# Kernel tuning notes

Hardware: AMD Instinct MI355X
Metric: run time of the kernel (lower is better)

Reference implementation:

```python
import jax, jax.numpy as jnp
import numpy as np

NUM_HEADS = 32
HEAD_DIM = 128
ROPE_THETA = 10000.0


def _rope_tables(seq_len, head_dim, theta):
    inv_freq = 1.0 / (theta ** (jnp.arange(0, head_dim, 2, dtype=jnp.float32) / head_dim))
    pos = jnp.arange(seq_len, dtype=jnp.float32)
    freqs = pos[:, None] * inv_freq[None, :]            # [S, hd/2]
    emb = jnp.concatenate([freqs, freqs], axis=-1)      # [S, hd]
    return jnp.cos(emb), jnp.sin(emb)


def _rotate_half(x):
    x1, x2 = jnp.split(x, 2, axis=-1)
    return jnp.concatenate([-x2, x1], axis=-1)


def _apply_rope(x, cos, sin):
    # x: [B, S, H, D]; cos/sin: [S, D] -> unsqueeze_dim=2 broadcasting
    c = cos[None, :, None, :]
    s = sin[None, :, None, :]
    return x * c + _rotate_half(x) * s


def setup_inputs() -> dict:
    key = jax.random.key(0)
    ks = jax.random.split(key, 6)
    hidden = 4096
    B, S = 2, 4096  # global sequence = world_size * local_seq (4 * 1024)
    hidden_states = jax.random.normal(ks[0], (B, S, hidden), dtype=jnp.float32)
    # original uses torch.rand (uniform); scaled by 0.02 for numerical sanity
    q_proj = jax.random.uniform(ks[1], (hidden, hidden), dtype=jnp.float32) * 0.02
    k_proj = jax.random.uniform(ks[2], (hidden, hidden), dtype=jnp.float32) * 0.02
    v_proj = jax.random.uniform(ks[3], (hidden, hidden), dtype=jnp.float32) * 0.02
    o_proj = jax.random.uniform(ks[4], (hidden, hidden), dtype=jnp.float32) * 0.02
    return {"hidden_states": hidden_states, "q_proj": q_proj, "k_proj": k_proj,
            "v_proj": v_proj, "o_proj": o_proj, "world_size": 4}


def _ring_attention(hidden_states, q_proj, k_proj, v_proj, o_proj, world_size):
    B, S, H = hidden_states.shape
    s_local = S // world_size
    nh, hd = NUM_HEADS, HEAD_DIM
    scale = 1.0 / np.sqrt(hd).astype(np.float32)

    # rank 0 holds the first sequence shard as its local hidden states
    hs_local = hidden_states[:, :s_local]
    q = (hs_local @ q_proj.T).reshape(B, s_local, nh, hd)
    k = (hidden_states @ k_proj.T).reshape(B, S, nh, hd)
    v = (hidden_states @ v_proj.T).reshape(B, S, nh, hd)

    cos, sin = _rope_tables(S, hd, ROPE_THETA)
    q = _apply_rope(q, cos[:s_local], sin[:s_local])   # rank0 positions 0..s_local-1
    k = _apply_rope(k, cos, sin)                       # global positions per shard

    # split into per-rank KV blocks; rank 0 receives blocks W-1, W-2, ..., 0
    k_blocks = k.reshape(B, world_size, s_local, nh, hd).transpose(1, 0, 2, 3, 4)[::-1]
    v_blocks = v.reshape(B, world_size, s_local, nh, hd).transpose(1, 0, 2, 3, 4)[::-1]

    def step(carry, kv):
        attn, max_lse, denom, lse_full = carry
        k_blk, v_blk = kv
        # memory_efficient_attention_partial: non-causal partial attention + lse
        s = jnp.einsum('bqhd,bkhd->bhqk', q, k_blk) * scale
        m = jnp.max(s, axis=-1)                          # [B,H,q]
        p = jnp.exp(s - m[..., None])
        l = jnp.sum(p, axis=-1)
        lse = (m + jnp.log(l)).transpose(0, 2, 1)        # [B,q,H]
        out = jnp.einsum('bhqk,bkhd->bqhd', p / l[..., None], v_blk)
        # online-softmax merge across ring steps
        new_max = jnp.maximum(max_lse, lse)
        old_adj = jnp.exp(max_lse - new_max)[..., None]
        new_adj = jnp.exp(lse - new_max)[..., None]
        denom = old_adj * denom + new_adj
        attn = old_adj * attn + new_adj * out
        lse_full = new_max + jnp.log(jnp.exp(lse_full - new_max) + jnp.exp(lse - new_max))
        return (attn, new_max, denom, lse_full), None

    init = (jnp.zeros((B, s_local, nh, hd), jnp.float32),
            jnp.full((B, s_local, nh), -jnp.inf, jnp.float32),
            jnp.zeros((B, s_local, nh, 1), jnp.float32),
            jnp.full((B, s_local, nh), -jnp.inf, jnp.float32))
    (attn, _, denom, _), _ = jax.lax.scan(step, init, (k_blocks, v_blocks))

    attn = attn / denom
    attn = attn.astype(jnp.float16).astype(jnp.float32)  # .half() in source
    attn = attn.reshape(B, s_local, nh * hd)
    return attn @ o_proj.T


def reference(hidden_states, q_proj, k_proj, v_proj, o_proj, world_size):
    return _ring_attention(hidden_states, q_proj, k_proj, v_proj, o_proj, world_size)
```

## Files before the change

kernel.cpp:

```cpp
#include <hip/hip_runtime.h>


using bf16x8 = __attribute__((ext_vector_type(8))) short;
using f32x4  = __attribute__((ext_vector_type(4))) float;

__device__ inline unsigned short f32_to_bf16_bits(float f) {
  unsigned int u = __float_as_uint(f);
  u += 0x7FFFu + ((u >> 16) & 1u);
  return (unsigned short)(u >> 16);
}
__device__ inline float bf16_bits_to_f32(unsigned short h) {
  return __uint_as_float(((unsigned int)h) << 16);
}

__device__ __forceinline__ void load_lds16(const unsigned short* g, unsigned short* l) {
  __builtin_amdgcn_global_load_lds(
      (const __attribute__((address_space(1))) void*)g,
      (__attribute__((address_space(3))) void*)l, 16, 0, 0);
}

__global__ void cast_f32_bf16(const float* __restrict__ in,
                              unsigned short* __restrict__ out, long n4) {
  long i = (long)blockIdx.x * blockDim.x + threadIdx.x;
  long stride = (long)gridDim.x * blockDim.x;
  for (; i < n4; i += stride) {
    float4 v = reinterpret_cast<const float4*>(in)[i];
    ushort4 o;
    o.x = f32_to_bf16_bits(v.x);
    o.y = f32_to_bf16_bits(v.y);
    o.z = f32_to_bf16_bits(v.z);
    o.w = f32_to_bf16_bits(v.w);
    reinterpret_cast<ushort4*>(out)[i] = o;
  }
}

__global__ void rope_tables(float* __restrict__ cos_t, float* __restrict__ sin_t) {
  int idx = blockIdx.x * 256 + threadIdx.x;
  if (idx >= 4096 * 64) return;
  int p = idx >> 6, i = idx & 63;
  float inv = __expf(-(float)i * (9.210340371976184f / 64.0f));
  float f = (float)p * inv;
  cos_t[idx] = cosf(f);
  sin_t[idx] = sinf(f);
}

__global__ void rope_apply_v(unsigned short* __restrict__ buf,
                             const float4* __restrict__ cos4,
                             const float4* __restrict__ sin4,
                             long nchunks, int pos_mask, float gain) {
  long idx = (long)blockIdx.x * 256 + threadIdx.x;
  if (idx >= nchunks) return;
  long tok = idx >> 8;
  int rem = (int)(idx & 255);
  int head = rem >> 3, c = rem & 7;
  int pos = (int)(tok & (long)pos_mask);
  float4 ct0 = cos4[pos * 16 + c * 2];
  float4 ct1 = cos4[pos * 16 + c * 2 + 1];
  float4 st0 = sin4[pos * 16 + c * 2];
  float4 st1 = sin4[pos * 16 + c * 2 + 1];
  float cs[8] = {ct0.x, ct0.y, ct0.z, ct0.w, ct1.x, ct1.y, ct1.z, ct1.w};
  float sn[8] = {st0.x, st0.y, st0.z, st0.w, st1.x, st1.y, st1.z, st1.w};
  long base = tok * 4096 + head * 128 + c * 8;
  bf16x8 x1 = *reinterpret_cast<const bf16x8*>(buf + base);
  bf16x8 x2 = *reinterpret_cast<const bf16x8*>(buf + base + 64);
  bf16x8 o1, o2;
#pragma unroll
  for (int j = 0; j < 8; j++) {
    float a = bf16_bits_to_f32((unsigned short)x1[j]);
    float b = bf16_bits_to_f32((unsigned short)x2[j]);
    o1[j] = (short)f32_to_bf16_bits((a * cs[j] - b * sn[j]) * gain);
    o2[j] = (short)f32_to_bf16_bits((b * cs[j] + a * sn[j]) * gain);
  }
  *reinterpret_cast<bf16x8*>(buf + base) = o1;
  *reinterpret_cast<bf16x8*>(buf + base + 64) = o2;
}

__device__ inline void storeC(float* p, float v) { *p = v; }
__device__ inline void storeC(unsigned short* p, float v) { *p = f32_to_bf16_bits(v); }

template <typename OUT_T>
__global__ __launch_bounds__(256) void gemm_bt(const unsigned short* __restrict__ A,
                                               const unsigned short* __restrict__ B,
                                               OUT_T* __restrict__ C,
                                               long Astride_z, long Cstride_z, int N) {
  __shared__ unsigned short As[128 * 32];
  __shared__ unsigned short Bs[128 * 32];
  const int tid = threadIdx.x;
  const int bn = blockIdx.x, bm = blockIdx.y, bz = blockIdx.z;
  const unsigned short* Ab = A + (long)bz * Astride_z + (long)bm * 128 * 4096;
  const unsigned short* Bb = B + (long)bn * 128 * 4096;
  OUT_T* Cb = C + (long)bz * Cstride_z + (long)bm * 128 * N + (long)bn * 128;

  const int lane = tid & 63;
  const int w = tid >> 6;
  const int wr = (w >> 1) * 64, wc = (w & 1) * 64;
  const int fr = lane & 15, fg = lane >> 4;

  f32x4 acc[4][4] = {};

  const int c0 = tid, c1 = tid + 256;
  const int rA0 = c0 >> 2, kc0 = c0 & 3;
  const int rA1 = c1 >> 2, kc1 = c1 & 3;

  for (int k0 = 0; k0 < 4096; k0 += 32) {
    load_lds16(Ab + (long)rA0 * 4096 + k0 + kc0 * 8, As + c0 * 8);
    load_lds16(Ab + (long)rA1 * 4096 + k0 + kc1 * 8, As + c1 * 8);
    load_lds16(Bb + (long)rA0 * 4096 + k0 + kc0 * 8, Bs + c0 * 8);
    load_lds16(Bb + (long)rA1 * 4096 + k0 + kc1 * 8, Bs + c1 * 8);
    __syncthreads();
    bf16x8 af[4], bfv[4];
#pragma unroll
    for (int m = 0; m < 4; m++)
      af[m] = *reinterpret_cast<const bf16x8*>(As + (wr + m * 16 + fr) * 32 + fg * 8);
#pragma unroll
    for (int n = 0; n < 4; n++)
      bfv[n] = *reinterpret_cast<const bf16x8*>(Bs + (wc + n * 16 + fr) * 32 + fg * 8);
#pragma unroll
    for (int m = 0; m < 4; m++)
#pragma unroll
      for (int n = 0; n < 4; n++)
        acc[m][n] = __builtin_amdgcn_mfma_f32_16x16x32_bf16(af[m], bfv[n], acc[m][n], 0, 0, 0);
    __syncthreads();
  }
#pragma unroll
  for (int m = 0; m < 4; m++)
#pragma unroll
    for (int n = 0; n < 4; n++)
#pragma unroll
      for (int r = 0; r < 4; r++) {
        int row = wr + m * 16 + fg * 4 + r;
        int col = wc + n * 16 + fr;
        storeC(Cb + (long)row * N + col, acc[m][n][r]);
      }
}

#define STG2(Gb, Lb, h, kc)                                                    \
  load_lds16((Gb) + (long)((h) * 128 + srow) * 4096 + sslot * 8 + (kc),        \
             (Lb) + tid * 8);                                                  \
  load_lds16((Gb) + (long)((h) * 128 + 64 + srow) * 4096 + sslot * 8 + (kc),   \
             (Lb) + 4096 + tid * 8);

#define MFMAQ(MH, NH)                                                          \
  _Pragma("unroll") for (int mi = 0; mi < 4; ++mi)                             \
    _Pragma("unroll") for (int ni = 0; ni < 2; ++ni)                           \
      _Pragma("unroll") for (int kk = 0; kk < 2; ++kk)                         \
        acc[(MH) * 4 + mi][(NH) * 2 + ni] =                                    \
            __builtin_amdgcn_mfma_f32_16x16x32_bf16(                           \
                a[mi][kk], b[(NH) * 2 + ni][kk],                               \
                acc[(MH) * 4 + mi][(NH) * 2 + ni], 0, 0, 0);

#define TILE(P, KC, MODE)                                                      \
  {                                                                            \
    const unsigned short* Ar = lds + wm * 16384 + (P) * 8192;                  \
    const unsigned short* Br =                                                 \
        lds + 32768 + (wn >> 1) * 16384 + (P) * 8192 + (wn & 1) * 4096;        \
    _Pragma("unroll") for (int mf = 0; mf < 4; ++mf) {                         \
      a[mf][0] = *reinterpret_cast<const bf16x8*>(Ar + mf * 1024 + ao0);       \
      a[mf][1] = *reinterpret_cast<const bf16x8*>(Ar + mf * 1024 + ao1);       \
    }                                                                          \
    _Pragma("unroll") for (int nf = 0; nf < 2; ++nf) {                         \
      b[nf][0] = *reinterpret_cast<const bf16x8*>(Br + nf * 1024 + ao0);       \
      b[nf][1] = *reinterpret_cast<const bf16x8*>(Br + nf * 1024 + ao1);       \
    }                                                                          \
    __builtin_amdgcn_s_setprio(1);                                             \
    MFMAQ(0, 0);                                                               \
    __builtin_amdgcn_s_setprio(0);                                             \
    _Pragma("unroll") for (int nf = 2; nf < 4; ++nf) {                         \
      b[nf][0] = *reinterpret_cast<const bf16x8*>(Br + nf * 1024 + ao0);       \
      b[nf][1] = *reinterpret_cast<const bf16x8*>(Br + nf * 1024 + ao1);       \
    }                                                                          \
    __builtin_amdgcn_s_setprio(1);                                             \
    MFMAQ(0, 1);                                                               \
    __builtin_amdgcn_s_setprio(0);                                             \
    asm volatile("s_waitcnt lgkmcnt(0)" ::: "memory");                         \
    asm volatile("s_barrier" ::: "memory");            \
    if ((MODE) == 0) {                                                         \
      STG2(Bg, lds + 32768 + (P) * 8192, 0, KC);                               \
      STG2(Bg, lds + 49152 + (P) * 8192, 1, KC);                               \
    }                                                                          \
    _Pragma("unroll") for (int mf = 0; mf < 4; ++mf) {                         \
      a[mf][0] = *reinterpret_cast<const bf16x8*>(Ar + (4 + mf) * 1024 + ao0); \
      a[mf][1] = *reinterpret_cast<const bf16x8*>(Ar + (4 + mf) * 1024 + ao1); \
    }                                                                          \
    __builtin_amdgcn_s_setprio(1);                                             \
    MFMAQ(1, 0);                                                               \
    __builtin_amdgcn_s_setprio(0);                                             \
    asm volatile("s_waitcnt lgkmcnt(0)" ::: "memory");                         \
    asm volatile("s_barrier" ::: "memory");            \
    if ((MODE) == 0) {                                                         \
      STG2(Ag, lds + (P) * 8192, 0, KC);                                       \
      STG2(Ag, lds + 16384 + (P) * 8192, 1, KC);                               \
    }                                                                          \
    __builtin_amdgcn_s_setprio(1);                                             \
    MFMAQ(1, 1);                                                               \
    __builtin_amdgcn_s_setprio(0);                                             \
    if ((MODE) == 0) asm volatile("s_waitcnt vmcnt(8)" ::: "memory");          \
    if ((MODE) == 1) asm volatile("s_waitcnt vmcnt(0)" ::: "memory");          \
    asm volatile("s_barrier" ::: "memory");       \
  }

template <typename OUT_T>
__global__ __launch_bounds__(512, 2) void gemm256(const unsigned short* __restrict__ A,
                                                  const unsigned short* __restrict__ B,
                                                  OUT_T* __restrict__ C,
                                                  long Astride_z, long Cstride_z, int N) {
  __shared__ unsigned short lds[65536];
  const int tid = threadIdx.x;
  const int bn = blockIdx.x, bm = blockIdx.y, bz = blockIdx.z;
  const unsigned short* Ag = A + (long)bz * Astride_z + (long)bm * 256 * 4096;
  const unsigned short* Bg = B + (long)bn * 256 * 4096;

  const int w = tid >> 6, lane = tid & 63;
  const int wm = w >> 2, wn = w & 3;
  const int fr = lane & 15, fg = lane >> 4;
  const int ao0 = fr * 64 + ((fg ^ (fr & 7)) * 8);
  const int ao1 = fr * 64 + (((4 + fg) ^ (fr & 7)) * 8);
  const int srow = tid >> 3;
  const int sslot = (tid & 7) ^ (srow & 7);

  f32x4 acc[8][4] = {};
  bf16x8 a[4][2], b[4][2];

  STG2(Ag, lds + 0, 0, 0);     STG2(Ag, lds + 16384, 1, 0);
  STG2(Bg, lds + 32768, 0, 0); STG2(Bg, lds + 49152, 1, 0);
  STG2(Ag, lds + 8192, 0, 64);  STG2(Ag, lds + 24576, 1, 64);
  STG2(Bg, lds + 40960, 0, 64); STG2(Bg, lds + 57344, 1, 64);
  asm volatile("s_waitcnt vmcnt(8)" ::: "memory");
  asm volatile("s_barrier" ::: "memory");

  for (int ti = 0; ti < 31; ++ti) {
    TILE(0, (2 * ti + 2) * 64, 0);
    TILE(1, (2 * ti + 3) * 64, 0);
  }
  TILE(0, 0, 1);
  TILE(1, 0, 2);

  OUT_T* Cb = C + (long)bz * Cstride_z + ((long)bm * 256) * N + bn * 256;
#pragma unroll
  for (int mf = 0; mf < 8; ++mf)
#pragma unroll
    for (int nf = 0; nf < 4; ++nf)
#pragma unroll
      for (int rr = 0; rr < 4; ++rr) {
        int row = wm * 128 + mf * 16 + fg * 4 + rr;
        int col = wn * 64 + nf * 16 + fr;
        storeC(Cb + (long)row * N + col, acc[mf][nf][rr]);
      }
}

#define AT_STAGE(P, kv)                                                        \
  _Pragma("unroll") for (int i = 0; i < 4; i++) {                              \
    int c = tid + 256 * i;                                                     \
    int key = c >> 4, s0 = c & 15;                                             \
    int Lg = s0 ^ (key & 15);                                                  \
    load_lds16(kbase + (long)((kv) + key) * 4096 + Lg * 8, &Ks[P][c * 8]);     \
  }                                                                            \
  _Pragma("unroll") for (int i = 0; i < 4; i++) {                              \
    int c = tid + 256 * i;                                                     \
    int f0 = c >> 3, s0 = c & 7;                                               \
    int Lg = s0 ^ (f0 & 7);                                                    \
    load_lds16(vbase + (long)f0 * 8192 + (kv) + Lg * 8, &Vl[P][c * 8]);        \
  }

__global__ __launch_bounds__(256) void attn_fwd(const unsigned short* __restrict__ qb,
                                                const unsigned short* __restrict__ kb,
                                                const unsigned short* __restrict__ vT,
                                                unsigned short* __restrict__ ob) {
  __shared__ unsigned short Ks[2][64 * 128];
  __shared__ unsigned short Vl[2][128 * 64];
  __shared__ unsigned short Ps[4][16 * 72];

  const int qt = blockIdx.x, h = blockIdx.y, b = blockIdx.z;
  const int tid = threadIdx.x, w = tid >> 6, lane = tid & 63;
  const int fr = lane & 15, fg = lane >> 4;

  const unsigned short* kbase = kb + (long)b * 4096 * 4096 + h * 128;
  const unsigned short* vbase = vT + (long)h * 128 * 8192 + (long)b * 4096;

  bf16x8 qf[4];
  {
    const unsigned short* qptr =
        qb + ((long)b * 1024 + qt * 64 + w * 16 + fr) * 4096 + h * 128 + fg * 8;
#pragma unroll
    for (int c = 0; c < 4; c++) qf[c] = *reinterpret_cast<const bf16x8*>(qptr + c * 32);
  }

  f32x4 outa[8] = {};
  float m_run[4], l_run[4];
#pragma unroll
  for (int r = 0; r < 4; r++) { m_run[r] = -1e30f; l_run[r] = 0.0f; }

  AT_STAGE(0, 0);
  asm volatile("s_waitcnt vmcnt(0)" ::: "memory");
  asm volatile("s_barrier" ::: "memory");

  for (int t = 0; t < 64; ++t) {
    const int cur = t & 1;
    if (t < 63) { AT_STAGE(cur ^ 1, (t + 1) * 64); }

    f32x4 sacc[4];
#pragma unroll
    for (int ks = 0; ks < 4; ks++) {
      f32x4 aq = {0.f, 0.f, 0.f, 0.f};
#pragma unroll
      for (int cc = 0; cc < 4; cc++) {
        bf16x8 kf = *reinterpret_cast<const bf16x8*>(
            &Ks[cur][(ks * 16 + fr) * 128 + (((cc * 4 + fg) ^ fr) & 15) * 8]);
        aq = __builtin_amdgcn_mfma_f32_16x16x32_bf16(qf[cc], kf, aq, 0, 0, 0);
      }
      sacc[ks] = aq;
    }

    float mx4[4];
#pragma unroll
    for (int r = 0; r < 4; r++) {
      float mx = fmaxf(fmaxf(sacc[0][r], sacc[1][r]), fmaxf(sacc[2][r], sacc[3][r]));
      mx = fmaxf(mx, __shfl_xor(mx, 1));
      mx = fmaxf(mx, __shfl_xor(mx, 2));
      mx = fmaxf(mx, __shfl_xor(mx, 4));
      mx = fmaxf(mx, __shfl_xor(mx, 8));
      mx4[r] = mx;
    }
    int need = 0;
#pragma unroll
    for (int r = 0; r < 4; r++) need |= (mx4[r] > m_run[r] + 11.5f) ? 1 : 0;
    if (__any(need)) {
#pragma unroll
      for (int r = 0; r < 4; r++) {
        float mnew = fmaxf(m_run[r], mx4[r]);
        float ef = exp2f(m_run[r] - mnew);
        l_run[r] *= ef;
        m_run[r] = mnew;
#pragma unroll
        for (int ds = 0; ds < 8; ds++) outa[ds][r] *= ef;
      }
    }
#pragma unroll
    for (int r = 0; r < 4; r++) {
      float sum = 0.f;
#pragma unroll
      for (int ks = 0; ks < 4; ks++) {
        float pv = exp2f(sacc[ks][r] - m_run[r]);
        Ps[w][(fg * 4 + r) * 72 + ks * 16 + fr] = f32_to_bf16_bits(pv);
        sum += pv;
      }
      l_run[r] += sum;
    }

#pragma unroll
    for (int c2 = 0; c2 < 2; c2++) {
      bf16x8 pf = *reinterpret_cast<const bf16x8*>(&Ps[w][fr * 72 + c2 * 32 + fg * 8]);
#pragma unroll
      for (int ds = 0; ds < 8; ds++) {
        int feat = ds * 16 + fr;
        int pch = ((c2 * 4 + fg) ^ (feat & 7)) & 7;
        bf16x8 vf = *reinterpret_cast<const bf16x8*>(&Vl[cur][feat * 64 + pch * 8]);
        outa[ds] = __builtin_amdgcn_mfma_f32_16x16x32_bf16(pf, vf, outa[ds], 0, 0, 0);
      }
    }

    if (t < 63) {
      asm volatile("s_waitcnt lgkmcnt(0)" ::: "memory");
      asm volatile("s_waitcnt vmcnt(0)" ::: "memory");
      asm volatile("s_barrier" ::: "memory");
    }
  }

#pragma unroll
  for (int r = 0; r < 4; r++) {
    float l = l_run[r];
    l += __shfl_xor(l, 1);
    l += __shfl_xor(l, 2);
    l += __shfl_xor(l, 4);
    l += __shfl_xor(l, 8);
    float inv = 1.0f / l;
    unsigned short* op =
        ob + ((long)b * 1024 + qt * 64 + w * 16 + fg * 4 + r) * 4096 + h * 128;
#pragma unroll
    for (int ds = 0; ds < 8; ds++) op[ds * 16 + fr] = f32_to_bf16_bits(outa[ds][r] * inv);
  }
}

extern "C" void kernel_launch(void* const* d_in, const int* in_sizes, int n_in,
                              void* d_out, int out_size, void* d_ws, size_t ws_size,
                              hipStream_t stream) {
  const float* hs = (const float*)d_in[0];
  const float* wq = (const float*)d_in[1];
  const float* wk = (const float*)d_in[2];
  const float* wv = (const float*)d_in[3];
  const float* wo = (const float*)d_in[4];
  float* out = (float*)d_out;

  const long hsN = 2L * 4096 * 4096;
  const long wN  = 4096L * 4096;

  unsigned short* hs_b = (unsigned short*)d_ws;
  unsigned short* wq_b = hs_b + hsN;
  unsigned short* wk_b = wq_b + wN;
  unsigned short* wv_b = wk_b + wN;
  unsigned short* wo_b = wv_b + wN;
  unsigned short* q_b  = wo_b + wN;
  unsigned short* k_b  = q_b + 2048L * 4096;
  unsigned short* vT_b = k_b + 8192L * 4096;
  unsigned short* at_b = vT_b + 8192L * 4096;
  float* cos_t = (float*)(at_b + 2048L * 4096);
  float* sin_t = cos_t + 4096 * 64;

  cast_f32_bf16<<<dim3(4096), dim3(256), 0, stream>>>(hs, hs_b, hsN / 4);
  cast_f32_bf16<<<dim3(2048), dim3(256), 0, stream>>>(wq, wq_b, wN / 4);
  cast_f32_bf16<<<dim3(2048), dim3(256), 0, stream>>>(wk, wk_b, wN / 4);
  cast_f32_bf16<<<dim3(2048), dim3(256), 0, stream>>>(wv, wv_b, wN / 4);
  cast_f32_bf16<<<dim3(2048), dim3(256), 0, stream>>>(wo, wo_b, wN / 4);

  rope_tables<<<dim3(1024), dim3(256), 0, stream>>>(cos_t, sin_t);

  gemm_bt<unsigned short><<<dim3(32, 8, 2), dim3(256), 0, stream>>>(
      hs_b, wq_b, q_b, 4096L * 4096, 1024L * 4096, 4096);
  gemm256<unsigned short><<<dim3(16, 16, 2), dim3(512), 0, stream>>>(
      hs_b, wk_b, k_b, 4096L * 4096, 4096L * 4096, 4096);
  gemm256<unsigned short><<<dim3(32, 16, 1), dim3(512), 0, stream>>>(
      wv_b, hs_b, vT_b, 0L, 0L, 8192);

  const float qgain = 0.08838834764831845f * 1.4426950408889634f;
  rope_apply_v<<<dim3(2048), dim3(256), 0, stream>>>(
      q_b, (const float4*)cos_t, (const float4*)sin_t, 2048L * 256, 1023, qgain);
  rope_apply_v<<<dim3(8192), dim3(256), 0, stream>>>(
      k_b, (const float4*)cos_t, (const float4*)sin_t, 8192L * 256, 4095, 1.0f);

  attn_fwd<<<dim3(16, 32, 2), dim3(256), 0, stream>>>(q_b, k_b, vT_b, at_b);

  gemm_bt<float><<<dim3(32, 16, 1), dim3(256), 0, stream>>>(
      at_b, wo_b, out, 0L, 0L, 4096);
}
```

Baseline: 1.078 ms.

## Load V fragments directly from global into registers and defer row-max shuffles

The attention kernel stops staging V tiles through shared memory. Each wave now reads its V MFMA operands straight from global memory into registers. These loads are issued early, before the softmax, so their latency can overlap with the exp work. The per-row max shuffle reduction now runs only when some lane's local max exceeds the running max by the rescale threshold, which removes cross-lane shuffles on most iterations. This frees LDS and cuts LDS traffic and bank pressure, but each of the four waves fetches the same V block on its own, so global/L2 traffic goes up and load latency may be exposed.

```diff
diff --git a/kernel.cpp b/kernel.cpp
--- a/kernel.cpp
+++ b/kernel.cpp
@@ -248,18 +248,12 @@
       }
 }
 
-#define AT_STAGE(P, kv)                                                        \
+#define KSTAGE(P, kv)                                                          \
   _Pragma("unroll") for (int i = 0; i < 4; i++) {                              \
     int c = tid + 256 * i;                                                     \
     int key = c >> 4, s0 = c & 15;                                             \
     int Lg = s0 ^ (key & 15);                                                  \
     load_lds16(kbase + (long)((kv) + key) * 4096 + Lg * 8, &Ks[P][c * 8]);     \
-  }                                                                            \
-  _Pragma("unroll") for (int i = 0; i < 4; i++) {                              \
-    int c = tid + 256 * i;                                                     \
-    int f0 = c >> 3, s0 = c & 7;                                               \
-    int Lg = s0 ^ (f0 & 7);                                                    \
-    load_lds16(vbase + (long)f0 * 8192 + (kv) + Lg * 8, &Vl[P][c * 8]);        \
   }
 
 __global__ __launch_bounds__(256) void attn_fwd(const unsigned short* __restrict__ qb,
@@ -267,7 +261,6 @@
                                                 const unsigned short* __restrict__ vT,
                                                 unsigned short* __restrict__ ob) {
   __shared__ unsigned short Ks[2][64 * 128];
-  __shared__ unsigned short Vl[2][128 * 64];
   __shared__ unsigned short Ps[4][16 * 72];
 
   const int qt = blockIdx.x, h = blockIdx.y, b = blockIdx.z;
@@ -275,7 +268,8 @@
   const int fr = lane & 15, fg = lane >> 4;
 
   const unsigned short* kbase = kb + (long)b * 4096 * 4096 + h * 128;
-  const unsigned short* vbase = vT + (long)h * 128 * 8192 + (long)b * 4096;
+  const unsigned short* vlane =
+      vT + (long)h * 1048576 + (long)b * 4096 + (long)fr * 8192 + fg * 8;
 
   bf16x8 qf[4];
   {
@@ -290,13 +284,14 @@
 #pragma unroll
   for (int r = 0; r < 4; r++) { m_run[r] = -1e30f; l_run[r] = 0.0f; }
 
-  AT_STAGE(0, 0);
+  KSTAGE(0, 0);
   asm volatile("s_waitcnt vmcnt(0)" ::: "memory");
   asm volatile("s_barrier" ::: "memory");
 
   for (int t = 0; t < 64; ++t) {
     const int cur = t & 1;
-    if (t < 63) { AT_STAGE(cur ^ 1, (t + 1) * 64); }
+    const long kv0 = (long)t * 64;
+    if (t < 63) { KSTAGE(cur ^ 1, (t + 1) * 64); }
 
     f32x4 sacc[4];
 #pragma unroll
@@ -311,23 +306,27 @@
       sacc[ks] = aq;
     }
 
-    float mx4[4];
+    bf16x8 vf0[8];
+#pragma unroll
+    for (int ds = 0; ds < 8; ds++)
+      vf0[ds] = *reinterpret_cast<const bf16x8*>(vlane + (long)ds * 131072 + kv0);
+
+    float mxl[4];
+    int need = 0;
 #pragma unroll
     for (int r = 0; r < 4; r++) {
-      float mx = fmaxf(fmaxf(sacc[0][r], sacc[1][r]), fmaxf(sacc[2][r], sacc[3][r]));
-      mx = fmaxf(mx, __shfl_xor(mx, 1));
-      mx = fmaxf(mx, __shfl_xor(mx, 2));
-      mx = fmaxf(mx, __shfl_xor(mx, 4));
-      mx = fmaxf(mx, __shfl_xor(mx, 8));
-      mx4[r] = mx;
-    }
-    int need = 0;
-#pragma unroll
-    for (int r = 0; r < 4; r++) need |= (mx4[r] > m_run[r] + 11.5f) ? 1 : 0;
+      mxl[r] = fmaxf(fmaxf(sacc[0][r], sacc[1][r]), fmaxf(sacc[2][r], sacc[3][r]));
+      need |= (mxl[r] > m_run[r] + 11.5f) ? 1 : 0;
+    }
     if (__any(need)) {
 #pragma unroll
       for (int r = 0; r < 4; r++) {
-        float mnew = fmaxf(m_run[r], mx4[r]);
+        float mx = mxl[r];
+        mx = fmaxf(mx, __shfl_xor(mx, 1));
+        mx = fmaxf(mx, __shfl_xor(mx, 2));
+        mx = fmaxf(mx, __shfl_xor(mx, 4));
+        mx = fmaxf(mx, __shfl_xor(mx, 8));
+        float mnew = fmaxf(m_run[r], mx);
         float ef = exp2f(m_run[r] - mnew);
         l_run[r] *= ef;
         m_run[r] = mnew;
@@ -347,21 +346,24 @@
       l_run[r] += sum;
     }
 
-#pragma unroll
-    for (int c2 = 0; c2 < 2; c2++) {
-      bf16x8 pf = *reinterpret_cast<const bf16x8*>(&Ps[w][fr * 72 + c2 * 32 + fg * 8]);
-#pragma unroll
-      for (int ds = 0; ds < 8; ds++) {
-        int feat = ds * 16 + fr;
-        int pch = ((c2 * 4 + fg) ^ (feat & 7)) & 7;
-        bf16x8 vf = *reinterpret_cast<const bf16x8*>(&Vl[cur][feat * 64 + pch * 8]);
-        outa[ds] = __builtin_amdgcn_mfma_f32_16x16x32_bf16(pf, vf, outa[ds], 0, 0, 0);
-      }
+    bf16x8 vf1[8];
+#pragma unroll
+    for (int ds = 0; ds < 8; ds++)
+      vf1[ds] = *reinterpret_cast<const bf16x8*>(vlane + (long)ds * 131072 + kv0 + 32);
+
+    {
+      bf16x8 pf0 = *reinterpret_cast<const bf16x8*>(&Ps[w][fr * 72 + fg * 8]);
+#pragma unroll
+      for (int ds = 0; ds < 8; ds++)
+        outa[ds] = __builtin_amdgcn_mfma_f32_16x16x32_bf16(pf0, vf0[ds], outa[ds], 0, 0, 0);
+      bf16x8 pf1 = *reinterpret_cast<const bf16x8*>(&Ps[w][fr * 72 + 32 + fg * 8]);
+#pragma unroll
+      for (int ds = 0; ds < 8; ds++)
+        outa[ds] = __builtin_amdgcn_mfma_f32_16x16x32_bf16(pf1, vf1[ds], outa[ds], 0, 0, 0);
     }
 
     if (t < 63) {
-      asm volatile("s_waitcnt lgkmcnt(0)" ::: "memory");
-      asm volatile("s_waitcnt vmcnt(0)" ::: "memory");
+      asm volatile("s_waitcnt vmcnt(0) lgkmcnt(0)" ::: "memory");
       asm volatile("s_barrier" ::: "memory");
     }
   }
```

New measurement: 1.320 ms. 1.22x slower.
